# Kernel tuning notes

Hardware: AMD Instinct MI355X
Metric: run time of the kernel (lower is better)

The kernel has to match this reference:

```python
import jax, jax.numpy as jnp
import numpy as np

NUM_HEADS = 32
NUM_KV_HEADS = 8
NUM_GROUPS = NUM_HEADS // NUM_KV_HEADS  # 4
HEAD_DIM = 64
HIDDEN = 2048
ROPE_THETA = 10000.0


def rotate_half(x):
    half = x.shape[-1] // 2
    x1, x2 = x[..., :half], x[..., half:]
    return jnp.concatenate([-x2, x1], axis=-1)


def rope_cos_sin(seq_len, dtype):
    inv_freq = 1.0 / (ROPE_THETA ** (jnp.arange(0, HEAD_DIM, 2, dtype=jnp.float32) / HEAD_DIM))
    pos = jnp.arange(seq_len, dtype=jnp.float32)
    freqs = jnp.outer(pos, inv_freq)          # [S, HEAD_DIM/2]
    emb = jnp.concatenate([freqs, freqs], axis=-1)  # [S, HEAD_DIM]
    return jnp.cos(emb).astype(dtype), jnp.sin(emb).astype(dtype)


def setup_inputs() -> dict:
    key = jax.random.key(0)
    k0, k1, k2, k3, k4 = jax.random.split(key, 5)
    B, S = 2, 2048
    scale = 0.02
    return {
        "hidden_states": jax.random.normal(k0, (B, S, HIDDEN), dtype=jnp.float32),
        "Wq": jax.random.normal(k1, (NUM_HEADS * HEAD_DIM, HIDDEN), dtype=jnp.float32) * scale,
        "Wk": jax.random.normal(k2, (NUM_KV_HEADS * HEAD_DIM, HIDDEN), dtype=jnp.float32) * scale,
        "Wv": jax.random.normal(k3, (NUM_KV_HEADS * HEAD_DIM, HIDDEN), dtype=jnp.float32) * scale,
        "Wo": jax.random.normal(k4, (HIDDEN, NUM_HEADS * HEAD_DIM), dtype=jnp.float32) * scale,
    }


def reference(hidden_states, Wq, Wk, Wv, Wo):
    B, S, _ = hidden_states.shape
    # projections (nn.Linear: x @ W.T)
    q = (hidden_states @ Wq.T).reshape(B, S, NUM_HEADS, HEAD_DIM).transpose(0, 2, 1, 3)
    k = (hidden_states @ Wk.T).reshape(B, S, NUM_KV_HEADS, HEAD_DIM).transpose(0, 2, 1, 3)
    v = (hidden_states @ Wv.T).reshape(B, S, NUM_KV_HEADS, HEAD_DIM).transpose(0, 2, 1, 3)

    cos, sin = rope_cos_sin(S, q.dtype)  # [S, HEAD_DIM]
    cos = cos[None, None]                # [1,1,S,HEAD_DIM]
    sin = sin[None, None]
    q = q * cos + rotate_half(q) * sin
    k = k * cos + rotate_half(k) * sin

    # GQA: repeat kv heads to match query heads (repeat_interleave on head dim)
    k = jnp.repeat(k, NUM_GROUPS, axis=1)  # [B, NUM_HEADS, S, HEAD_DIM]
    v = jnp.repeat(v, NUM_GROUPS, axis=1)

    scale = 1.0 / jnp.sqrt(jnp.asarray(HEAD_DIM, dtype=q.dtype))
    scores = jnp.einsum('bhqd,bhkd->bhqk', q, k) * scale  # [B,H,S,S]
    causal = jnp.tril(jnp.ones((S, S), dtype=bool))
    scores = jnp.where(causal[None, None], scores, jnp.asarray(-jnp.inf, dtype=scores.dtype))
    attn = jax.nn.softmax(scores, axis=-1)
    out = jnp.einsum('bhqk,bhkd->bhqd', attn, v)           # [B,H,S,D]
    out = out.transpose(0, 2, 1, 3).reshape(B, S, NUM_HEADS * HEAD_DIM)
    return out @ Wo.T
```

## Files before the change

### kernel.cpp

```cpp
#include <hip/hip_runtime.h>

#define S_LEN 2048
#define BATCH 2
#define NH 32
#define NKV 8
#define HD 64
#define HID 2048
#define NTOK (BATCH * S_LEN)
#define NQKV 3072
#define SC_Q 0.18033688011112042f

typedef __attribute__((ext_vector_type(8))) __bf16 bf16x8;
typedef __attribute__((ext_vector_type(4))) float f32x4;

__device__ inline ushort f2b(float f) {
    union { float f; unsigned u; } x{f};
    unsigned r = (x.u + 0x7fff + ((x.u >> 16) & 1)) >> 16;
    return (ushort)r;
}
__device__ inline float ex2(float x) { return __builtin_amdgcn_exp2f(x); }

__global__ __launch_bounds__(256) void cvt_all(const float* __restrict__ hidden,
                                               const float* __restrict__ Wq,
                                               const float* __restrict__ Wk,
                                               const float* __restrict__ Wv,
                                               const float* __restrict__ Wo,
                                               ushort* __restrict__ hb,
                                               ushort* __restrict__ wqkv,
                                               ushort* __restrict__ wo) {
    int bid = blockIdx.x;
    const float* src;
    ushort* dst;
    int off;
    if (bid < 8192)        { src = hidden; dst = hb;                              off = bid; }
    else if (bid < 12288)  { src = Wq;     dst = wqkv;                            off = bid - 8192; }
    else if (bid < 13312)  { src = Wk;     dst = wqkv + (size_t)2048 * 2048;      off = bid - 12288; }
    else if (bid < 14336)  { src = Wv;     dst = wqkv + (size_t)2560 * 2048;      off = bid - 13312; }
    else                   { src = Wo;     dst = wo;                              off = bid - 14336; }
    size_t i = (size_t)off * 256 + threadIdx.x;
    float4 v = reinterpret_cast<const float4*>(src)[i];
    ushort4 o;
    o.x = f2b(v.x); o.y = f2b(v.y); o.z = f2b(v.z); o.w = f2b(v.w);
    reinterpret_cast<ushort4*>(dst)[i] = o;
}

__device__ inline void gl_lds16(const void* g, void* l) {
    __builtin_amdgcn_global_load_lds((const __attribute__((address_space(1))) void*)g,
                                     (__attribute__((address_space(3))) void*)l, 16, 0, 0);
}

template<int WF32, int ROPE>
__global__ __launch_bounds__(256) void gemm_bt(const ushort* __restrict__ A,
                                               const ushort* __restrict__ B,
                                               void* __restrict__ C,
                                               ushort* __restrict__ Kd,
                                               ushort* __restrict__ Vd,
                                               int M, int N, int K) {
    __shared__ __align__(16) ushort As[128 * 64];
    __shared__ __align__(16) ushort Bs[128 * 64];
    const int tid = threadIdx.x, lane = tid & 63, w = tid >> 6;
    const int wr = w >> 1, wc = w & 1, l15 = lane & 15, lg = lane >> 4;

    const int nbx = gridDim.x;
    int lid = blockIdx.y * nbx + blockIdx.x;
    const int cpx = (nbx * gridDim.y) >> 3;
    int swz = (lid & 7) * cpx + (lid >> 3);
    const int m0 = (swz / nbx) * 128, n0 = (swz % nbx) * 128;

    const int lsw = ((lane & 7) ^ (lane >> 3)) * 8;
    const ushort* Ag = A + (size_t)(m0 + w * 8 + (lane >> 3)) * K + lsw;
    const ushort* Bg = B + (size_t)(n0 + w * 8 + (lane >> 3)) * K + lsw;
    ushort* lA = As + w * 512;
    ushort* lB = Bs + w * 512;

    f32x4 acc[4][4] = {};

    for (int k0 = 0; k0 < K; k0 += 64) {
        __syncthreads();
#pragma unroll
        for (int j = 0; j < 4; j++) {
            gl_lds16(Ag + (size_t)(j * 32) * K + k0, lA + j * 2048);
            gl_lds16(Bg + (size_t)(j * 32) * K + k0, lB + j * 2048);
        }
        __syncthreads();

        const char* pa = (const char*)As + (wr * 64 + l15) * 128;
        const char* pb = (const char*)Bs + (wc * 64 + l15) * 128;
        const int sw = (l15 & 7) * 16;
        bf16x8 af[2][4], bff[2][4];
#pragma unroll
        for (int i = 0; i < 4; i++)
#pragma unroll
            for (int ks = 0; ks < 2; ks++) {
                const int po = (ks * 64 + lg * 16) ^ sw;
                af[ks][i]  = *(const bf16x8*)(pa + i * 2048 + po);
                bff[ks][i] = *(const bf16x8*)(pb + i * 2048 + po);
            }
#pragma unroll
        for (int ks = 0; ks < 2; ks++)
#pragma unroll
            for (int i = 0; i < 4; i++)
#pragma unroll
                for (int j = 0; j < 4; j++)
                    acc[i][j] = __builtin_amdgcn_mfma_f32_16x16x32_bf16(af[ks][i], bff[ks][j], acc[i][j], 0, 0, 0);
    }

    const int mr = m0 + wr * 64 + lg * 4, nc = n0 + wc * 64 + l15;

    if (!ROPE) {
#pragma unroll
        for (int i = 0; i < 4; i++)
#pragma unroll
            for (int j = 0; j < 4; j++)
#pragma unroll
                for (int r = 0; r < 4; r++) {
                    size_t row = mr + i * 16 + r, col = nc + j * 16;
                    if (WF32) ((float*)C)[row * N + col] = acc[i][j][r];
                    else      ((ushort*)C)[row * N + col] = f2b(acc[i][j][r]);
                }
        return;
    }

    const int hq = (n0 + wc * 64) >> 6;
    if (hq < 40) {
        const bool isQ = hq < 32;
        const float fd0 = ex2(-(float)l15 * 0.4152410118609203f);
        const float fd1 = fd0 * 0.01f;
#pragma unroll
        for (int i = 0; i < 4; i++)
#pragma unroll
            for (int r = 0; r < 4; r++) {
                float pos = (float)((mr + i * 16 + r) & (S_LEN - 1));
#pragma unroll
                for (int jj = 0; jj < 2; jj++) {
                    float ang = pos * (jj ? fd1 : fd0);
                    float sv, cv;
                    __sincosf(ang, &sv, &cv);
                    float x1 = acc[i][jj][r], x2 = acc[i][jj + 2][r];
                    float y0 = x1 * cv - x2 * sv;
                    float y1 = x2 * cv + x1 * sv;
                    if (isQ) { y0 *= SC_Q; y1 *= SC_Q; }
                    acc[i][jj][r] = y0;
                    acc[i][jj + 2][r] = y1;
                }
            }
    }
    ushort* dst;
    int dstride, colb;
    if (hq < 32)      { dst = (ushort*)C; dstride = 2048; colb = nc; }
    else if (hq < 40) { dst = Kd;         dstride = 512;  colb = nc - 2048; }
    else              { dst = Vd;         dstride = 512;  colb = nc - 2560; }
#pragma unroll
    for (int i = 0; i < 4; i++)
#pragma unroll
        for (int j = 0; j < 4; j++)
#pragma unroll
            for (int r = 0; r < 4; r++) {
                size_t row = mr + i * 16 + r;
                dst[row * dstride + colb + j * 16] = f2b(acc[i][j][r]);
            }
}

__global__ __launch_bounds__(256) void transpose_v(const ushort* __restrict__ V,
                                                   ushort* __restrict__ Vt) {
    __shared__ ushort tile[32][33];
    int bz = blockIdx.z, b = bz >> 3, kvh = bz & 7;
    int s0 = blockIdx.x * 32, d0 = blockIdx.y * 32;
    int tx = threadIdx.x & 31, ty = threadIdx.x >> 5;
#pragma unroll
    for (int i = 0; i < 4; i++)
        tile[ty + i * 8][tx] = V[(size_t)(b * S_LEN + s0 + ty + i * 8) * 512 + kvh * 64 + d0 + tx];
    __syncthreads();
#pragma unroll
    for (int i = 0; i < 4; i++)
        Vt[((size_t)((b * 8 + kvh) * 64 + d0 + ty + i * 8)) * S_LEN + s0 + tx] = tile[tx][ty + i * 8];
}

__global__ __launch_bounds__(256) void attn_k(const ushort* __restrict__ Q,
                                              const ushort* __restrict__ Kc,
                                              const ushort* __restrict__ Vt,
                                              ushort* __restrict__ O) {
    __shared__ __align__(16) ushort K_lds[2][4096];
    __shared__ __align__(16) ushort V_lds[2][4096];
    const int lane = threadIdx.x & 63, w = threadIdx.x >> 6;
    const int l15 = lane & 15, lg = lane >> 4;

    int lid = blockIdx.y * 16 + blockIdx.x;
    int swz = (lid & 7) * 128 + (lid >> 3);
    const int bxs = swz & 15;
    const int bh = swz >> 4;
    const int b = bh >> 5, h = bh & 31, kvh = h >> 2;

    const ushort* kSrc[2];
    const ushort* vSrc[2];
    int dstU[2];
#pragma unroll
    for (int j = 0; j < 2; j++) {
        int u = w * 2 + j;
        int row = u * 8 + (lane >> 3);
        int po = (lane & 7) * 16;
        int fr = ((row & 3) | (((row >> 3) & 1) << 2)) << 4;
        int dus = (po ^ fr) >> 1;
        kSrc[j] = Kc + (size_t)(b * S_LEN + row) * 512 + kvh * 64 + dus;
        vSrc[j] = Vt + ((size_t)((b * 8 + kvh) * 64 + row)) * S_LEN + dus;
        dstU[j] = u * 512;
    }

    int fr_k = ((l15 & 3) | (((l15 >> 2) & 1) << 2)) << 4;
    int kbase = 1024 * (l15 >> 2) + 128 * (l15 & 3) + ((lg * 16) ^ (fr_k & 48));
    int k6 = (fr_k >> 6) & 1;
    int kb0 = kbase + 64 * k6, kb1 = kbase + 64 * (1 - k6);
    int fr_v = ((l15 & 3) | (((l15 >> 3) & 1) << 2)) << 4;
    int vbase = 128 * l15 + ((lg * 16) ^ (fr_v & 48));
    int v6 = (fr_v >> 6) & 1;
    int vb0 = vbase + 64 * v6, vb1 = vbase + 64 * (1 - v6);

    bf16x8 onesf;
#pragma unroll
    for (int i = 0; i < 8; i++) onesf[i] = (__bf16)1.0f;

    const int ktA = bxs, ktB = 31 - bxs;
    const int q0A = bxs * 64 + w * 16, q0B = (31 - bxs) * 64 + w * 16;
    const int qrowA = q0A + l15, qrowB = q0B + l15;

    const ushort* qpA = Q + (size_t)(b * S_LEN + qrowA) * HID + h * 64 + lg * 8;
    const ushort* qpB = Q + (size_t)(b * S_LEN + qrowB) * HID + h * 64 + lg * 8;
    bf16x8 qfA0 = *(const bf16x8*)qpA, qfA1 = *(const bf16x8*)(qpA + 32);
    bf16x8 qfB0 = *(const bf16x8*)qpB, qfB1 = *(const bf16x8*)(qpB + 32);

    f32x4 aoA[4] = {}, aoB[4] = {};
    f32x4 lsumA = {}, lsumB = {};

#pragma unroll
    for (int j = 0; j < 2; j++) {
        gl_lds16(kSrc[j], &K_lds[0][dstU[j]]);
        gl_lds16(vSrc[j], &V_lds[0][dstU[j]]);
    }
    __syncthreads();
    int cur = 0;

    for (int kt = 0; kt <= ktB; ++kt) {
        const int kn = kt << 6;
        if (kt < ktB) {
            const int kn2 = kn + 64;
#pragma unroll
            for (int j = 0; j < 2; j++) {
                gl_lds16(kSrc[j] + (size_t)kn2 * 512, &K_lds[cur ^ 1][dstU[j]]);
                gl_lds16(vSrc[j] + kn2, &V_lds[cur ^ 1][dstU[j]]);
            }
        }

        const char* Kt = (const char*)K_lds[cur];
        const char* Vl = (const char*)V_lds[cur];
        const bool aAct = (kt <= ktA);

        bf16x8 kf0[4], kf1[4];
#pragma unroll
        for (int kc = 0; kc < 4; kc++) {
            const int kcst = 4096 * (kc >> 1) + 512 * (kc & 1);
            kf0[kc] = *(const bf16x8*)(Kt + kb0 + kcst);
            kf1[kc] = *(const bf16x8*)(Kt + kb1 + kcst);
        }

        f32x4 sB[4], sA[4];
#pragma unroll
        for (int kc = 0; kc < 4; kc++) {
            f32x4 z = {};
            z = __builtin_amdgcn_mfma_f32_16x16x32_bf16(kf0[kc], qfB0, z, 0, 0, 0);
            z = __builtin_amdgcn_mfma_f32_16x16x32_bf16(kf1[kc], qfB1, z, 0, 0, 0);
            sB[kc] = z;
        }
        if (aAct) {
#pragma unroll
            for (int kc = 0; kc < 4; kc++) {
                f32x4 z = {};
                z = __builtin_amdgcn_mfma_f32_16x16x32_bf16(kf0[kc], qfA0, z, 0, 0, 0);
                z = __builtin_amdgcn_mfma_f32_16x16x32_bf16(kf1[kc], qfA1, z, 0, 0, 0);
                sA[kc] = z;
            }
        }

        if (kt == ktB) {
#pragma unroll
            for (int kc = 0; kc < 4; kc++)
#pragma unroll
                for (int r = 0; r < 4; r++) {
                    int kv = kn + ((kc >> 1) << 5) + (lg << 3) + ((kc & 1) << 2) + r;
                    sB[kc][r] = (kv <= qrowB) ? sB[kc][r] : -INFINITY;
                }
        }
        if (kt == ktA) {
#pragma unroll
            for (int kc = 0; kc < 4; kc++)
#pragma unroll
                for (int r = 0; r < 4; r++) {
                    int kv = kn + ((kc >> 1) << 5) + (lg << 3) + ((kc & 1) << 2) + r;
                    sA[kc][r] = (kv <= qrowA) ? sA[kc][r] : -INFINITY;
                }
        }

        bf16x8 pB0, pB1, pA0, pA1;
#pragma unroll
        for (int r = 0; r < 4; r++) {
            pB0[r]     = (__bf16)ex2(sB[0][r]);
            pB0[4 + r] = (__bf16)ex2(sB[1][r]);
            pB1[r]     = (__bf16)ex2(sB[2][r]);
            pB1[4 + r] = (__bf16)ex2(sB[3][r]);
        }
        if (aAct) {
#pragma unroll
            for (int r = 0; r < 4; r++) {
                pA0[r]     = (__bf16)ex2(sA[0][r]);
                pA0[4 + r] = (__bf16)ex2(sA[1][r]);
                pA1[r]     = (__bf16)ex2(sA[2][r]);
                pA1[4 + r] = (__bf16)ex2(sA[3][r]);
            }
        }

        lsumB = __builtin_amdgcn_mfma_f32_16x16x32_bf16(pB0, onesf, lsumB, 0, 0, 0);
        lsumB = __builtin_amdgcn_mfma_f32_16x16x32_bf16(pB1, onesf, lsumB, 0, 0, 0);
        if (aAct) {
            lsumA = __builtin_amdgcn_mfma_f32_16x16x32_bf16(pA0, onesf, lsumA, 0, 0, 0);
            lsumA = __builtin_amdgcn_mfma_f32_16x16x32_bf16(pA1, onesf, lsumA, 0, 0, 0);
        }

#pragma unroll
        for (int dt = 0; dt < 4; dt++) {
            bf16x8 vf0 = *(const bf16x8*)(Vl + vb0 + dt * 2048);
            bf16x8 vf1 = *(const bf16x8*)(Vl + vb1 + dt * 2048);
            aoB[dt] = __builtin_amdgcn_mfma_f32_16x16x32_bf16(pB0, vf0, aoB[dt], 0, 0, 0);
            aoB[dt] = __builtin_amdgcn_mfma_f32_16x16x32_bf16(pB1, vf1, aoB[dt], 0, 0, 0);
            if (aAct) {
                aoA[dt] = __builtin_amdgcn_mfma_f32_16x16x32_bf16(pA0, vf0, aoA[dt], 0, 0, 0);
                aoA[dt] = __builtin_amdgcn_mfma_f32_16x16x32_bf16(pA1, vf1, aoA[dt], 0, 0, 0);
            }
        }

        __syncthreads();
        cur ^= 1;
    }

    float invA[4], invB[4];
#pragma unroll
    for (int r = 0; r < 4; r++) { invA[r] = 1.0f / lsumA[r]; invB[r] = 1.0f / lsumB[r]; }
    ushort* obA = O + (size_t)(b * S_LEN + q0A + lg * 4) * HID + h * 64 + l15;
    ushort* obB = O + (size_t)(b * S_LEN + q0B + lg * 4) * HID + h * 64 + l15;
#pragma unroll
    for (int dt = 0; dt < 4; dt++)
#pragma unroll
        for (int r = 0; r < 4; r++) {
            union { __bf16 h; ushort u; } cA{(__bf16)(aoA[dt][r] * invA[r])};
            union { __bf16 h; ushort u; } cB{(__bf16)(aoB[dt][r] * invB[r])};
            obA[(size_t)r * HID + dt * 16] = cA.u;
            obB[(size_t)r * HID + dt * 16] = cB.u;
        }
}

extern "C" void kernel_launch(void* const* d_in, const int* in_sizes, int n_in,
                              void* d_out, int out_size, void* d_ws, size_t ws_size,
                              hipStream_t stream) {
    const float* hidden = (const float*)d_in[0];
    const float* Wq = (const float*)d_in[1];
    const float* Wk = (const float*)d_in[2];
    const float* Wv = (const float*)d_in[3];
    const float* Wo = (const float*)d_in[4];

    char* ws = (char*)d_ws;
    size_t off = 0;
    auto alloc = [&](size_t bytes) -> void* {
        void* p = ws + off;
        off += (bytes + 255) & ~(size_t)255;
        return p;
    };
    ushort* hb   = (ushort*)alloc((size_t)NTOK * HID * 2);
    ushort* wqkv = (ushort*)alloc((size_t)NQKV * 2048 * 2);
    ushort* wo   = (ushort*)alloc((size_t)2048 * 2048 * 2);
    ushort* Qb   = (ushort*)alloc((size_t)NTOK * 2048 * 2);
    ushort* Kb   = (ushort*)alloc((size_t)NTOK * 512 * 2);
    ushort* Vb   = (ushort*)alloc((size_t)NTOK * 512 * 2);
    ushort* Vtb  = (ushort*)alloc((size_t)NTOK * 512 * 2);
    ushort* AO   = (ushort*)alloc((size_t)NTOK * 2048 * 2);

    cvt_all<<<18432, 256, 0, stream>>>(hidden, Wq, Wk, Wv, Wo, hb, wqkv, wo);

    gemm_bt<0, 1><<<dim3(24, 32), 256, 0, stream>>>(hb, wqkv, Qb, Kb, Vb, NTOK, NQKV, 2048);

    transpose_v<<<dim3(S_LEN / 32, 2, BATCH * NKV), 256, 0, stream>>>(Vb, Vtb);

    attn_k<<<dim3(16, BATCH * NH), 256, 0, stream>>>(Qb, Kb, Vtb, AO);

    gemm_bt<1, 0><<<dim3(16, 32), 256, 0, stream>>>(AO, wo, d_out, nullptr, nullptr, NTOK, 2048, 2048);
}
```

Baseline: 185.4 us.

## Triple-buffer K/V in attention and pair adjacent query tiles per block

The attention kernel now keeps three K/V LDS buffers and prefetches two tiles ahead, using explicit vmcnt waits and a raw s_barrier instead of __syncthreads. Work is reassigned so each block handles two adjacent 64-row query tiles that share K/V tiles, processing a balanced pair (pp and 15-pp) in two sequential halves. The grid is halved to 512 blocks. This aims to hide global-to-LDS latency and reuse K tiles across two query tiles, at the cost of more LDS, fewer blocks and the load-balancing tradeoffs of sequential halves.

```diff
diff --git a/kernel.cpp b/kernel.cpp
--- a/kernel.cpp
+++ b/kernel.cpp
@@ -180,15 +180,15 @@
                                               const ushort* __restrict__ Kc,
                                               const ushort* __restrict__ Vt,
                                               ushort* __restrict__ O) {
-    __shared__ __align__(16) ushort K_lds[2][4096];
-    __shared__ __align__(16) ushort V_lds[2][4096];
+    __shared__ __align__(16) ushort K_lds[3][4096];
+    __shared__ __align__(16) ushort V_lds[3][4096];
     const int lane = threadIdx.x & 63, w = threadIdx.x >> 6;
     const int l15 = lane & 15, lg = lane >> 4;
 
-    int lid = blockIdx.y * 16 + blockIdx.x;
-    int swz = (lid & 7) * 128 + (lid >> 3);
-    const int bxs = swz & 15;
-    const int bh = swz >> 4;
+    int lid = blockIdx.y * 8 + blockIdx.x;
+    int swz = (lid & 7) * 64 + (lid >> 3);
+    const int ps = swz & 7;
+    const int bh = swz >> 3;
     const int b = bh >> 5, h = bh & 31, kvh = h >> 2;
 
     const ushort* kSrc[2];
@@ -219,141 +219,154 @@
 #pragma unroll
     for (int i = 0; i < 8; i++) onesf[i] = (__bf16)1.0f;
 
-    const int ktA = bxs, ktB = 31 - bxs;
-    const int q0A = bxs * 64 + w * 16, q0B = (31 - bxs) * 64 + w * 16;
-    const int qrowA = q0A + l15, qrowB = q0B + l15;
-
-    const ushort* qpA = Q + (size_t)(b * S_LEN + qrowA) * HID + h * 64 + lg * 8;
-    const ushort* qpB = Q + (size_t)(b * S_LEN + qrowB) * HID + h * 64 + lg * 8;
-    bf16x8 qfA0 = *(const bf16x8*)qpA, qfA1 = *(const bf16x8*)(qpA + 32);
-    bf16x8 qfB0 = *(const bf16x8*)qpB, qfB1 = *(const bf16x8*)(qpB + 32);
-
-    f32x4 aoA[4] = {}, aoB[4] = {};
-    f32x4 lsumA = {}, lsumB = {};
-
-#pragma unroll
-    for (int j = 0; j < 2; j++) {
-        gl_lds16(kSrc[j], &K_lds[0][dstU[j]]);
-        gl_lds16(vSrc[j], &V_lds[0][dstU[j]]);
-    }
-    __syncthreads();
-    int cur = 0;
-
-    for (int kt = 0; kt <= ktB; ++kt) {
-        const int kn = kt << 6;
-        if (kt < ktB) {
-            const int kn2 = kn + 64;
-#pragma unroll
-            for (int j = 0; j < 2; j++) {
-                gl_lds16(kSrc[j] + (size_t)kn2 * 512, &K_lds[cur ^ 1][dstU[j]]);
-                gl_lds16(vSrc[j] + kn2, &V_lds[cur ^ 1][dstU[j]]);
-            }
+    for (int half = 0; half < 2; ++half) {
+        const int pp = half ? (15 - ps) : ps;
+        const int q0A = pp * 128 + w * 16, q0B = q0A + 64;
+        const int qrowA = q0A + l15, qrowB = q0B + l15;
+        const int ktA = 2 * pp, ktB = 2 * pp + 1;
+
+        const ushort* qpA = Q + (size_t)(b * S_LEN + qrowA) * HID + h * 64 + lg * 8;
+        const ushort* qpB = Q + (size_t)(b * S_LEN + qrowB) * HID + h * 64 + lg * 8;
+        bf16x8 qfA0 = *(const bf16x8*)qpA, qfA1 = *(const bf16x8*)(qpA + 32);
+        bf16x8 qfB0 = *(const bf16x8*)qpB, qfB1 = *(const bf16x8*)(qpB + 32);
+        asm volatile("s_waitcnt vmcnt(0)" ::: "memory");
+
+        f32x4 aoA[4] = {}, aoB[4] = {};
+        f32x4 lsumA = {}, lsumB = {};
+
+        int i0 = 0, i1 = 1, i2 = 2;
+#pragma unroll
+        for (int j = 0; j < 2; j++) {
+            gl_lds16(kSrc[j], &K_lds[0][dstU[j]]);
+            gl_lds16(vSrc[j], &V_lds[0][dstU[j]]);
         }
-
-        const char* Kt = (const char*)K_lds[cur];
-        const char* Vl = (const char*)V_lds[cur];
-        const bool aAct = (kt <= ktA);
-
-        bf16x8 kf0[4], kf1[4];
-#pragma unroll
-        for (int kc = 0; kc < 4; kc++) {
-            const int kcst = 4096 * (kc >> 1) + 512 * (kc & 1);
-            kf0[kc] = *(const bf16x8*)(Kt + kb0 + kcst);
-            kf1[kc] = *(const bf16x8*)(Kt + kb1 + kcst);
+#pragma unroll
+        for (int j = 0; j < 2; j++) {
+            gl_lds16(kSrc[j] + (size_t)64 * 512, &K_lds[1][dstU[j]]);
+            gl_lds16(vSrc[j] + 64, &V_lds[1][dstU[j]]);
         }
 
-        f32x4 sB[4], sA[4];
-#pragma unroll
-        for (int kc = 0; kc < 4; kc++) {
-            f32x4 z = {};
-            z = __builtin_amdgcn_mfma_f32_16x16x32_bf16(kf0[kc], qfB0, z, 0, 0, 0);
-            z = __builtin_amdgcn_mfma_f32_16x16x32_bf16(kf1[kc], qfB1, z, 0, 0, 0);
-            sB[kc] = z;
-        }
-        if (aAct) {
+        for (int kt = 0; kt <= ktB; ++kt) {
+            const int kn = kt << 6;
+            if (kt < ktB) asm volatile("s_waitcnt vmcnt(4)" ::: "memory");
+            else          asm volatile("s_waitcnt vmcnt(0)" ::: "memory");
+            __builtin_amdgcn_s_barrier();
+
+            if (kt + 2 <= ktB) {
+                const int kn2 = kn + 128;
+#pragma unroll
+                for (int j = 0; j < 2; j++) {
+                    gl_lds16(kSrc[j] + (size_t)kn2 * 512, &K_lds[i2][dstU[j]]);
+                    gl_lds16(vSrc[j] + kn2, &V_lds[i2][dstU[j]]);
+                }
+            }
+
+            const char* Kt = (const char*)&K_lds[i0][0];
+            const char* Vl = (const char*)&V_lds[i0][0];
+            const bool aAct = (kt <= ktA);
+
+            bf16x8 kf0[4], kf1[4];
+#pragma unroll
+            for (int kc = 0; kc < 4; kc++) {
+                const int kcst = 4096 * (kc >> 1) + 512 * (kc & 1);
+                kf0[kc] = *(const bf16x8*)(Kt + kb0 + kcst);
+                kf1[kc] = *(const bf16x8*)(Kt + kb1 + kcst);
+            }
+
+            f32x4 sB[4], sA[4];
 #pragma unroll
             for (int kc = 0; kc < 4; kc++) {
                 f32x4 z = {};
-                z = __builtin_amdgcn_mfma_f32_16x16x32_bf16(kf0[kc], qfA0, z, 0, 0, 0);
-                z = __builtin_amdgcn_mfma_f32_16x16x32_bf16(kf1[kc], qfA1, z, 0, 0, 0);
-                sA[kc] = z;
-            }
+                z = __builtin_amdgcn_mfma_f32_16x16x32_bf16(kf0[kc], qfB0, z, 0, 0, 0);
+                z = __builtin_amdgcn_mfma_f32_16x16x32_bf16(kf1[kc], qfB1, z, 0, 0, 0);
+                sB[kc] = z;
+            }
+            if (aAct) {
+#pragma unroll
+                for (int kc = 0; kc < 4; kc++) {
+                    f32x4 z = {};
+                    z = __builtin_amdgcn_mfma_f32_16x16x32_bf16(kf0[kc], qfA0, z, 0, 0, 0);
+                    z = __builtin_amdgcn_mfma_f32_16x16x32_bf16(kf1[kc], qfA1, z, 0, 0, 0);
+                    sA[kc] = z;
+                }
+            }
+
+            if (kt == ktB) {
+#pragma unroll
+                for (int kc = 0; kc < 4; kc++)
+#pragma unroll
+                    for (int r = 0; r < 4; r++) {
+                        int kv = kn + ((kc >> 1) << 5) + (lg << 3) + ((kc & 1) << 2) + r;
+                        sB[kc][r] = (kv <= qrowB) ? sB[kc][r] : -INFINITY;
+                    }
+            }
+            if (kt == ktA) {
+#pragma unroll
+                for (int kc = 0; kc < 4; kc++)
+#pragma unroll
+                    for (int r = 0; r < 4; r++) {
+                        int kv = kn + ((kc >> 1) << 5) + (lg << 3) + ((kc & 1) << 2) + r;
+                        sA[kc][r] = (kv <= qrowA) ? sA[kc][r] : -INFINITY;
+                    }
+            }
+
+            bf16x8 pB0, pB1, pA0, pA1;
+#pragma unroll
+            for (int r = 0; r < 4; r++) {
+                pB0[r]     = (__bf16)ex2(sB[0][r]);
+                pB0[4 + r] = (__bf16)ex2(sB[1][r]);
+                pB1[r]     = (__bf16)ex2(sB[2][r]);
+                pB1[4 + r] = (__bf16)ex2(sB[3][r]);
+            }
+            if (aAct) {
+#pragma unroll
+                for (int r = 0; r < 4; r++) {
+                    pA0[r]     = (__bf16)ex2(sA[0][r]);
+                    pA0[4 + r] = (__bf16)ex2(sA[1][r]);
+                    pA1[r]     = (__bf16)ex2(sA[2][r]);
+                    pA1[4 + r] = (__bf16)ex2(sA[3][r]);
+                }
+            }
+
+            lsumB = __builtin_amdgcn_mfma_f32_16x16x32_bf16(pB0, onesf, lsumB, 0, 0, 0);
+            lsumB = __builtin_amdgcn_mfma_f32_16x16x32_bf16(pB1, onesf, lsumB, 0, 0, 0);
+            if (aAct) {
+                lsumA = __builtin_amdgcn_mfma_f32_16x16x32_bf16(pA0, onesf, lsumA, 0, 0, 0);
+                lsumA = __builtin_amdgcn_mfma_f32_16x16x32_bf16(pA1, onesf, lsumA, 0, 0, 0);
+            }
+
+#pragma unroll
+            for (int dt = 0; dt < 4; dt++) {
+                bf16x8 vf0 = *(const bf16x8*)(Vl + vb0 + dt * 2048);
+                bf16x8 vf1 = *(const bf16x8*)(Vl + vb1 + dt * 2048);
+                aoB[dt] = __builtin_amdgcn_mfma_f32_16x16x32_bf16(pB0, vf0, aoB[dt], 0, 0, 0);
+                aoB[dt] = __builtin_amdgcn_mfma_f32_16x16x32_bf16(pB1, vf1, aoB[dt], 0, 0, 0);
+                if (aAct) {
+                    aoA[dt] = __builtin_amdgcn_mfma_f32_16x16x32_bf16(pA0, vf0, aoA[dt], 0, 0, 0);
+                    aoA[dt] = __builtin_amdgcn_mfma_f32_16x16x32_bf16(pA1, vf1, aoA[dt], 0, 0, 0);
+                }
+            }
+
+            int t = i0; i0 = i1; i1 = i2; i2 = t;
         }
 
-        if (kt == ktB) {
-#pragma unroll
-            for (int kc = 0; kc < 4; kc++)
-#pragma unroll
-                for (int r = 0; r < 4; r++) {
-                    int kv = kn + ((kc >> 1) << 5) + (lg << 3) + ((kc & 1) << 2) + r;
-                    sB[kc][r] = (kv <= qrowB) ? sB[kc][r] : -INFINITY;
-                }
-        }
-        if (kt == ktA) {
-#pragma unroll
-            for (int kc = 0; kc < 4; kc++)
-#pragma unroll
-                for (int r = 0; r < 4; r++) {
-                    int kv = kn + ((kc >> 1) << 5) + (lg << 3) + ((kc & 1) << 2) + r;
-                    sA[kc][r] = (kv <= qrowA) ? sA[kc][r] : -INFINITY;
-                }
-        }
-
-        bf16x8 pB0, pB1, pA0, pA1;
-#pragma unroll
-        for (int r = 0; r < 4; r++) {
-            pB0[r]     = (__bf16)ex2(sB[0][r]);
-            pB0[4 + r] = (__bf16)ex2(sB[1][r]);
-            pB1[r]     = (__bf16)ex2(sB[2][r]);
-            pB1[4 + r] = (__bf16)ex2(sB[3][r]);
-        }
-        if (aAct) {
+        float invA[4], invB[4];
+#pragma unroll
+        for (int r = 0; r < 4; r++) { invA[r] = 1.0f / lsumA[r]; invB[r] = 1.0f / lsumB[r]; }
+        ushort* obA = O + (size_t)(b * S_LEN + q0A + lg * 4) * HID + h * 64 + l15;
+        ushort* obB = O + (size_t)(b * S_LEN + q0B + lg * 4) * HID + h * 64 + l15;
+#pragma unroll
+        for (int dt = 0; dt < 4; dt++)
 #pragma unroll
             for (int r = 0; r < 4; r++) {
-                pA0[r]     = (__bf16)ex2(sA[0][r]);
-                pA0[4 + r] = (__bf16)ex2(sA[1][r]);
-                pA1[r]     = (__bf16)ex2(sA[2][r]);
-                pA1[4 + r] = (__bf16)ex2(sA[3][r]);
-            }
-        }
-
-        lsumB = __builtin_amdgcn_mfma_f32_16x16x32_bf16(pB0, onesf, lsumB, 0, 0, 0);
-        lsumB = __builtin_amdgcn_mfma_f32_16x16x32_bf16(pB1, onesf, lsumB, 0, 0, 0);
-        if (aAct) {
-            lsumA = __builtin_amdgcn_mfma_f32_16x16x32_bf16(pA0, onesf, lsumA, 0, 0, 0);
-            lsumA = __builtin_amdgcn_mfma_f32_16x16x32_bf16(pA1, onesf, lsumA, 0, 0, 0);
-        }
-
-#pragma unroll
-        for (int dt = 0; dt < 4; dt++) {
-            bf16x8 vf0 = *(const bf16x8*)(Vl + vb0 + dt * 2048);
-            bf16x8 vf1 = *(const bf16x8*)(Vl + vb1 + dt * 2048);
-            aoB[dt] = __builtin_amdgcn_mfma_f32_16x16x32_bf16(pB0, vf0, aoB[dt], 0, 0, 0);
-            aoB[dt] = __builtin_amdgcn_mfma_f32_16x16x32_bf16(pB1, vf1, aoB[dt], 0, 0, 0);
-            if (aAct) {
-                aoA[dt] = __builtin_amdgcn_mfma_f32_16x16x32_bf16(pA0, vf0, aoA[dt], 0, 0, 0);
-                aoA[dt] = __builtin_amdgcn_mfma_f32_16x16x32_bf16(pA1, vf1, aoA[dt], 0, 0, 0);
-            }
-        }
-
-        __syncthreads();
-        cur ^= 1;
+                union { __bf16 h; ushort u; } cA{(__bf16)(aoA[dt][r] * invA[r])};
+                union { __bf16 h; ushort u; } cB{(__bf16)(aoB[dt][r] * invB[r])};
+                obA[(size_t)r * HID + dt * 16] = cA.u;
+                obB[(size_t)r * HID + dt * 16] = cB.u;
+            }
+
+        __builtin_amdgcn_s_barrier();
     }
-
-    float invA[4], invB[4];
-#pragma unroll
-    for (int r = 0; r < 4; r++) { invA[r] = 1.0f / lsumA[r]; invB[r] = 1.0f / lsumB[r]; }
-    ushort* obA = O + (size_t)(b * S_LEN + q0A + lg * 4) * HID + h * 64 + l15;
-    ushort* obB = O + (size_t)(b * S_LEN + q0B + lg * 4) * HID + h * 64 + l15;
-#pragma unroll
-    for (int dt = 0; dt < 4; dt++)
-#pragma unroll
-        for (int r = 0; r < 4; r++) {
-            union { __bf16 h; ushort u; } cA{(__bf16)(aoA[dt][r] * invA[r])};
-            union { __bf16 h; ushort u; } cB{(__bf16)(aoB[dt][r] * invB[r])};
-            obA[(size_t)r * HID + dt * 16] = cA.u;
-            obB[(size_t)r * HID + dt * 16] = cB.u;
-        }
 }
 
 extern "C" void kernel_launch(void* const* d_in, const int* in_sizes, int n_in,
@@ -387,7 +400,7 @@
 
     transpose_v<<<dim3(S_LEN / 32, 2, BATCH * NKV), 256, 0, stream>>>(Vb, Vtb);
 
-    attn_k<<<dim3(16, BATCH * NH), 256, 0, stream>>>(Qb, Kb, Vtb, AO);
+    attn_k<<<dim3(8, BATCH * NH), 256, 0, stream>>>(Qb, Kb, Vtb, AO);
 
     gemm_bt<1, 0><<<dim3(16, 32), 256, 0, stream>>>(AO, wo, d_out, nullptr, nullptr, NTOK, 2048, 2048);
 }
```

After: 169.0 us. -8.9%, faster.
